# Optimization experiments

Measured on AMD Instinct MI355X. Metric: run time of the kernel, lower is better.

The kernel has to match this reference:

```python
import jax, jax.numpy as jnp
import numpy as np

DIM = 256
WS = 7
NUM_HEADS = 8
NW = 4096


def _relative_position_index(ws: int) -> jnp.ndarray:
    coords = jnp.stack(jnp.meshgrid(jnp.arange(ws), jnp.arange(ws), indexing='ij'))  # [2, ws, ws]
    flat = coords.reshape(2, -1)                                # [2, N]
    rel = flat[:, :, None] - flat[:, None, :]                   # [2, N, N]
    rel = rel.transpose(1, 2, 0) + (ws - 1)                     # [N, N, 2]
    rel = rel.at[:, :, 0].multiply(2 * ws - 1)
    return rel.sum(-1).astype(jnp.int32)                        # [N, N]


def setup_inputs() -> dict:
    key = jax.random.key(0)
    ks = jax.random.split(key, 7)
    N = WS * WS
    x_win = jax.random.normal(ks[0], (NW, N, DIM), dtype=jnp.float32)
    attn_mask = jnp.zeros((NW, N, N), dtype=jnp.float32)
    w_qkv = jax.random.normal(ks[1], (3 * DIM, DIM), dtype=jnp.float32) * (1.0 / np.sqrt(DIM))
    b_qkv = jax.random.normal(ks[2], (3 * DIM,), dtype=jnp.float32) * 0.02
    w_proj = jax.random.normal(ks[3], (DIM, DIM), dtype=jnp.float32) * (1.0 / np.sqrt(DIM))
    b_proj = jax.random.normal(ks[4], (DIM,), dtype=jnp.float32) * 0.02
    bias_table = jax.random.normal(ks[5], ((2 * WS - 1) * (2 * WS - 1), NUM_HEADS), dtype=jnp.float32)
    rel_index = _relative_position_index(WS)
    return {
        'x_win': x_win, 'attn_mask': attn_mask,
        'w_qkv': w_qkv, 'b_qkv': b_qkv,
        'w_proj': w_proj, 'b_proj': b_proj,
        'bias_table': bias_table, 'rel_index': rel_index,
    }


def reference(x_win, attn_mask, w_qkv, b_qkv, w_proj, b_proj, bias_table, rel_index):
    nW, N, C = x_win.shape
    H = bias_table.shape[-1]
    head_dim = C // H
    scale = 1.0 / np.sqrt(head_dim).astype(np.float32)

    # QKV projection (eqx.nn.Linear: y = W x + b)
    qkv = jnp.einsum('wnc,oc->wno', x_win, w_qkv) + b_qkv      # [nW, N, 3C]
    q, k, v = jnp.split(qkv, 3, axis=-1)

    def to_heads(t):
        return t.reshape(nW, N, H, head_dim).transpose(0, 2, 1, 3)  # [nW, H, N, d]

    q, k, v = to_heads(q), to_heads(k), to_heads(v)

    attn = jnp.einsum('whnd,whmd->whnm', q * scale, k)          # [nW, H, N, N]

    # Gathered relative position bias -> [H, N, N]
    bias = bias_table[rel_index.reshape(-1)].reshape(N, N, H).transpose(2, 0, 1)
    attn = attn + bias[None, :, :, :] + attn_mask[:, None, :, :]
    attn = jax.nn.softmax(attn, axis=-1)

    out = jnp.einsum('whnm,whmd->whnd', attn, v)                # [nW, H, N, d]
    out = out.transpose(0, 2, 1, 3).reshape(nW, N, C)
    out = jnp.einsum('wnc,oc->wno', out, w_proj) + b_proj
    return out
```

## Files before the change

kernel.cpp:

```cpp
#include <hip/hip_runtime.h>
#include <hip/hip_bf16.h>

typedef __bf16 bf16;
typedef bf16 bf16x4 __attribute__((ext_vector_type(4)));
typedef bf16 bf16x8 __attribute__((ext_vector_type(8)));
typedef float f32x4 __attribute__((ext_vector_type(4)));

#define MFMA16(a, b, c) __builtin_amdgcn_mfma_f32_16x16x32_bf16((a), (b), (c), 0, 0, 0)

constexpr int kN = 49, kC = 256;
constexpr float kScale = 0.17677669529663687f;

constexpr int WQKV_OFF = 0;
constexpr int WPROJ_OFF = 393216;
constexpr int BIAS_OFF = 524288;
constexpr int BQKV_OFF = 601120;

constexpr int XB_OFF = 0;
constexpr int QK_OFF = 25600;
constexpr int QS = 400;
constexpr int LDS_BYTES = 76800;

__global__ void prep_kernel(const float* __restrict__ w_qkv, const float* __restrict__ b_qkv,
                            const float* __restrict__ w_proj, const float* __restrict__ bias_table,
                            const int* __restrict__ rel_index, char* __restrict__ ws) {
  int i = blockIdx.x * 256 + threadIdx.x;
  bf16* wqkvb = (bf16*)(ws + WQKV_OFF);
  bf16* wprojb = (bf16*)(ws + WPROJ_OFF);
  float* biasx = (float*)(ws + BIAS_OFF);
  float* bqs = (float*)(ws + BQKV_OFF);
  if (i < 196608) {
    float v = w_qkv[i];
    if (i < 65536) v *= kScale;
    wqkvb[i] = (bf16)v;
  } else if (i < 262144) {
    int j = i - 196608;
    wprojb[j] = (bf16)w_proj[j];
  } else if (i < 281352) {
    int j = i - 262144;
    int h = j / 2401, nm = j - h * 2401;
    int mm = nm / 49, nn = nm - mm * 49;
    biasx[j] = bias_table[rel_index[nn * 49 + mm] * 8 + h];
  } else if (i < 282120) {
    int j = i - 281352;
    bqs[j] = b_qkv[j] * (j < 256 ? kScale : 1.0f);
  }
}

__global__ __launch_bounds__(256, 2) void attn_kernel(
    const float* __restrict__ x, const float* __restrict__ mask, const float* __restrict__ b_proj,
    const char* __restrict__ ws, float* __restrict__ out) {
  extern __shared__ char smem[];
  bf16* xb = (bf16*)(smem + XB_OFF);
  bf16* qk = (bf16*)(smem + QK_OFF);
  float* outf = (float*)(smem + QK_OFF);

  const bf16* wqkvb = (const bf16*)(ws + WQKV_OFF);
  const bf16* wprojb = (const bf16*)(ws + WPROJ_OFF);
  const float* biasx = (const float*)(ws + BIAS_OFF);
  const float* bqs = (const float*)(ws + BQKV_OFF);

  const int tid = threadIdx.x;
  const int w = blockIdx.x;
  const int lane = tid & 63;
  const int wave = tid >> 6;
  const int g = lane >> 4;
  const int c = lane & 15;

  const float* xw = x + (size_t)w * (kN * kC);

#pragma unroll
  for (int it = 0; it < 13; ++it) {
    int idx = it * 256 + tid;
    if (idx < 3136) {
      int n = idx >> 6, c4 = (idx & 63) << 2;
      float4 v = ((const float4*)xw)[idx];
      bf16x4 b4;
      b4[0] = (bf16)v.x; b4[1] = (bf16)v.y; b4[2] = (bf16)v.z; b4[3] = (bf16)v.w;
      *(bf16x4*)(xb + ((c4 >> 3) * QS + n * 8 + (c4 & 7))) = b4;
    }
  }
  __syncthreads();

  for (int t = 0; t < 8; ++t) {
    int ot = wave * 8 + t;
    const bf16* ab = wqkvb + (ot * 16 + c) * 256 + g * 8;
    bf16x8 afr[8];
#pragma unroll
    for (int ks = 0; ks < 8; ++ks) afr[ks] = *(const bf16x8*)(ab + ks * 32);
    f32x4 acc[4] = {};
#pragma unroll
    for (int ks = 0; ks < 8; ++ks) {
      const bf16* bb = xb + (ks * 4 + g) * QS + c * 8;
#pragma unroll
      for (int nt = 0; nt < 4; ++nt) {
        bf16x8 bfr = *(const bf16x8*)(bb + nt * 128);
        acc[nt] = MFMA16(afr[ks], bfr, acc[nt]);
      }
    }
    int ob = ot * 16 + g * 4;
    float bq0 = bqs[ob], bq1 = bqs[ob + 1], bq2 = bqs[ob + 2], bq3 = bqs[ob + 3];
    int oc = ob >> 3, olow = ob & 7;
#pragma unroll
    for (int nt = 0; nt < 4; ++nt) {
      int n = nt * 16 + c;
      if (n < 50) {
        bool ok = (n < 49);
        bf16x4 pk;
        pk[0] = ok ? (bf16)(acc[nt][0] + bq0) : (bf16)0.f;
        pk[1] = ok ? (bf16)(acc[nt][1] + bq1) : (bf16)0.f;
        pk[2] = ok ? (bf16)(acc[nt][2] + bq2) : (bf16)0.f;
        pk[3] = ok ? (bf16)(acc[nt][3] + bq3) : (bf16)0.f;
        *(bf16x4*)(qk + (oc * QS + n * 8 + olow)) = pk;
      }
    }
  }

  bf16x8 va[2][2][2];
  for (int t = 0; t < 4; ++t) {
    int ct = wave * 4 + t;
    int o = 512 + ct * 16 + c;
    const bf16* bb = wqkvb + o * 256 + g * 8;
    bf16x8 bfr[8];
#pragma unroll
    for (int ks = 0; ks < 8; ++ks) bfr[ks] = *(const bf16x8*)(bb + ks * 32);
    f32x4 acc[4] = {};
#pragma unroll
    for (int ks = 0; ks < 8; ++ks) {
      const bf16* abL = xb + (ks * 4 + g) * QS + c * 8;
#pragma unroll
      for (int mt = 0; mt < 4; ++mt) {
        bf16x8 afr = *(const bf16x8*)(abL + mt * 128);
        acc[mt] = MFMA16(afr, bfr[ks], acc[mt]);
      }
    }
    float bv = bqs[o];
#pragma unroll
    for (int mt = 0; mt < 4; ++mt) {
      acc[mt][0] += bv; acc[mt][1] += bv; acc[mt][2] += bv; acc[mt][3] += bv;
    }
    int hh = t >> 1, dt = t & 1;
    int base = ((g & 1) * 2) * 16 + c;
#pragma unroll
    for (int ks = 0; ks < 2; ++ks) {
      f32x4 aL = acc[2 * ks], aH = acc[2 * ks + 1];
      float e[8];
#pragma unroll
      for (int i = 0; i < 4; ++i) {
        float xA = __shfl(aL[i], base), yA = __shfl(aH[i], base);
        float xB = __shfl(aL[i], base + 16), yB = __shfl(aH[i], base + 16);
        e[i] = (g < 2) ? xA : yA;
        e[4 + i] = (g < 2) ? xB : yB;
      }
      bf16x8 f;
#pragma unroll
      for (int j = 0; j < 8; ++j) {
        int m = ks * 32 + g * 8 + j;
        f[j] = (m < 49) ? (bf16)e[j] : (bf16)0.f;
      }
      va[hh][dt][ks] = f;
    }
  }
  __syncthreads();

  const int h0 = wave * 2;
  const float* mk = mask + (size_t)w * 2401;

#pragma unroll
  for (int hh = 0; hh < 2; ++hh) {
    int h = h0 + hh;
    const float* bhT = biasx + h * 2401;

    bf16x8 qa[4], kb[4];
#pragma unroll
    for (int rt = 0; rt < 4; ++rt) {
      int n = rt * 16 + c; n = n > 49 ? 49 : n;
      qa[rt] = *(const bf16x8*)(qk + ((h * 4 + g) * QS + n * 8));
    }
#pragma unroll
    for (int mt = 0; mt < 4; ++mt) {
      int m = mt * 16 + c; m = m > 49 ? 49 : m;
      kb[mt] = *(const bf16x8*)(qk + ((32 + h * 4 + g) * QS + m * 8));
    }

    f32x4 s[4][4] = {};
#pragma unroll
    for (int mt = 0; mt < 4; ++mt)
#pragma unroll
      for (int nt = 0; nt < 4; ++nt) s[mt][nt] = MFMA16(kb[mt], qa[nt], s[mt][nt]);

    f32x4 oacc[2][4] = {};
#pragma unroll
    for (int nt = 0; nt < 4; ++nt) {
      int n = nt * 16 + c;
      int nc = n > 48 ? 48 : n;
      bool nok = (n < 49);
      float vals[4][4];
#pragma unroll
      for (int mt = 0; mt < 4; ++mt)
#pragma unroll
        for (int i = 0; i < 4; ++i) {
          int m = mt * 16 + g * 4 + i;
          int mc2 = m > 48 ? 48 : m;
          float bv = bhT[mc2 * 49 + nc];
          float mv = mk[nc * 49 + mc2];
          vals[mt][i] = (nok && m < 49) ? (s[mt][nt][i] + bv + mv) : -1e30f;
        }
      float mx = vals[0][0];
#pragma unroll
      for (int mt = 0; mt < 4; ++mt)
#pragma unroll
        for (int i = 0; i < 4; ++i) mx = fmaxf(mx, vals[mt][i]);
      mx = fmaxf(mx, __shfl_xor(mx, 16));
      mx = fmaxf(mx, __shfl_xor(mx, 32));
      float p_[4][4];
      float sum = 0.f;
#pragma unroll
      for (int mt = 0; mt < 4; ++mt)
#pragma unroll
        for (int i = 0; i < 4; ++i) {
          float pv = __expf(vals[mt][i] - mx);
          p_[mt][i] = pv;
          sum += pv;
        }
      sum += __shfl_xor(sum, 16);
      sum += __shfl_xor(sum, 32);
      float rinv = nok ? (1.0f / sum) : 0.0f;
#pragma unroll
      for (int mt = 0; mt < 4; ++mt)
#pragma unroll
        for (int i = 0; i < 4; ++i) p_[mt][i] *= rinv;

#pragma unroll
      for (int ks = 0; ks < 2; ++ks) {
        float e[8];
#pragma unroll
        for (int j = 0; j < 8; ++j) {
          int src = ((g & 1) * 2 + (j >> 2)) * 16 + c;
          float vA = __shfl(p_[2 * ks][j & 3], src);
          float vB = __shfl(p_[2 * ks + 1][j & 3], src);
          e[j] = (g < 2) ? vA : vB;
        }
        bf16x8 f;
#pragma unroll
        for (int j = 0; j < 8; ++j) f[j] = (bf16)e[j];
#pragma unroll
        for (int dt = 0; dt < 2; ++dt) oacc[dt][nt] = MFMA16(va[hh][dt][ks], f, oacc[dt][nt]);
      }
    }

#pragma unroll
    for (int dt = 0; dt < 2; ++dt) {
      int cb = h * 32 + dt * 16 + g * 4;
      int cc = cb >> 3, clow = cb & 7;
#pragma unroll
      for (int nt = 0; nt < 4; ++nt) {
        int n = nt * 16 + c;
        if (n < 49) {
          bf16x4 pk;
          pk[0] = (bf16)oacc[dt][nt][0]; pk[1] = (bf16)oacc[dt][nt][1];
          pk[2] = (bf16)oacc[dt][nt][2]; pk[3] = (bf16)oacc[dt][nt][3];
          *(bf16x4*)(xb + (cc * QS + n * 8 + clow)) = pk;
        }
      }
    }
  }
  __syncthreads();

  for (int t = 0; t < 4; ++t) {
    int ct = wave * 4 + t;
    const bf16* bb = wprojb + (ct * 16 + c) * 256 + g * 8;
    bf16x8 bfr[8];
#pragma unroll
    for (int ks = 0; ks < 8; ++ks) bfr[ks] = *(const bf16x8*)(bb + ks * 32);
    f32x4 acc[4] = {};
#pragma unroll
    for (int ks = 0; ks < 8; ++ks) {
      const bf16* abL = xb + (ks * 4 + g) * QS + c * 8;
#pragma unroll
      for (int mt = 0; mt < 4; ++mt) {
        bf16x8 afr = *(const bf16x8*)(abL + mt * 128);
        acc[mt] = MFMA16(afr, bfr[ks], acc[mt]);
      }
    }
    float bp = b_proj[ct * 16 + c];
    int co = ct * 16 + c, q = co >> 2, c3 = co & 3;
#pragma unroll
    for (int mt = 0; mt < 4; ++mt) {
#pragma unroll
      for (int i = 0; i < 4; ++i) {
        int n = mt * 16 + g * 4 + i;
        if (n < 49) outf[n * 256 + ((q ^ (n & 15)) << 2) + c3] = acc[mt][i] + bp;
      }
    }
  }
  __syncthreads();

  float4* outw4 = (float4*)(out + (size_t)w * (kN * kC));
  const float4* outf4 = (const float4*)outf;
#pragma unroll
  for (int it = 0; it < 13; ++it) {
    int f = it * 256 + tid;
    if (f < 3136) {
      int n = f >> 6, q = f & 63;
      outw4[f] = outf4[n * 64 + (q ^ (n & 15))];
    }
  }
}

extern "C" void kernel_launch(void* const* d_in, const int* in_sizes, int n_in,
                              void* d_out, int out_size, void* d_ws, size_t ws_size,
                              hipStream_t stream) {
  const float* x = (const float*)d_in[0];
  const float* mask = (const float*)d_in[1];
  const float* w_qkv = (const float*)d_in[2];
  const float* b_qkv = (const float*)d_in[3];
  const float* w_proj = (const float*)d_in[4];
  const float* b_proj = (const float*)d_in[5];
  const float* bias_table = (const float*)d_in[6];
  const int* rel_index = (const int*)d_in[7];
  float* out = (float*)d_out;
  char* ws = (char*)d_ws;

  (void)in_sizes; (void)n_in; (void)out_size; (void)ws_size;

  hipFuncSetAttribute((const void*)attn_kernel, hipFuncAttributeMaxDynamicSharedMemorySize,
                      LDS_BYTES);

  prep_kernel<<<1103, 256, 0, stream>>>(w_qkv, b_qkv, w_proj, bias_table, rel_index, ws);
  attn_kernel<<<4096, 256, LDS_BYTES, stream>>>(x, mask, b_proj, ws, out);
}
```

Before: 431.0 us.

## Fuse per-head QKV projection into attention to shrink LDS and raise occupancy

Each wave now computes the Q and K projections for its own heads directly into registers through lane shuffles, so Q/K never go through LDS. The attention output gets its own LDS buffer, and the output projection is staged in two column halves that reuse the x buffer. Together these cut LDS from 76.8KB to about 51KB, which allows the launch bound to rise from 2 to 3 blocks per CU. In exchange there is more register pressure, extra shuffles, and an additional pair of barriers in the output stage.

```diff
diff --git a/kernel.cpp b/kernel.cpp
--- a/kernel.cpp
+++ b/kernel.cpp
@@ -8,7 +8,6 @@
 
 #define MFMA16(a, b, c) __builtin_amdgcn_mfma_f32_16x16x32_bf16((a), (b), (c), 0, 0, 0)
 
-constexpr int kN = 49, kC = 256;
 constexpr float kScale = 0.17677669529663687f;
 
 constexpr int WQKV_OFF = 0;
@@ -16,10 +15,10 @@
 constexpr int BIAS_OFF = 524288;
 constexpr int BQKV_OFF = 601120;
 
-constexpr int XB_OFF = 0;
-constexpr int QK_OFF = 25600;
+constexpr int A_OFF = 0;
+constexpr int B_OFF = 25600;
 constexpr int QS = 400;
-constexpr int LDS_BYTES = 76800;
+constexpr int LDS_BYTES = 51456;
 
 __global__ void prep_kernel(const float* __restrict__ w_qkv, const float* __restrict__ b_qkv,
                             const float* __restrict__ w_proj, const float* __restrict__ bias_table,
@@ -47,13 +46,13 @@
   }
 }
 
-__global__ __launch_bounds__(256, 2) void attn_kernel(
+__global__ __launch_bounds__(256, 3) void attn_kernel(
     const float* __restrict__ x, const float* __restrict__ mask, const float* __restrict__ b_proj,
     const char* __restrict__ ws, float* __restrict__ out) {
   extern __shared__ char smem[];
-  bf16* xb = (bf16*)(smem + XB_OFF);
-  bf16* qk = (bf16*)(smem + QK_OFF);
-  float* outf = (float*)(smem + QK_OFF);
+  bf16* xb = (bf16*)(smem + A_OFF);
+  bf16* ao = (bf16*)(smem + B_OFF);
+  float* outf = (float*)(smem + A_OFF);
 
   const bf16* wqkvb = (const bf16*)(ws + WQKV_OFF);
   const bf16* wprojb = (const bf16*)(ws + WPROJ_OFF);
@@ -67,7 +66,7 @@
   const int g = lane >> 4;
   const int c = lane & 15;
 
-  const float* xw = x + (size_t)w * (kN * kC);
+  const float* xw = x + (size_t)w * 12544;
 
 #pragma unroll
   for (int it = 0; it < 13; ++it) {
@@ -82,119 +81,117 @@
   }
   __syncthreads();
 
-  for (int t = 0; t < 8; ++t) {
-    int ot = wave * 8 + t;
-    const bf16* ab = wqkvb + (ot * 16 + c) * 256 + g * 8;
-    bf16x8 afr[8];
-#pragma unroll
-    for (int ks = 0; ks < 8; ++ks) afr[ks] = *(const bf16x8*)(ab + ks * 32);
-    f32x4 acc[4] = {};
-#pragma unroll
-    for (int ks = 0; ks < 8; ++ks) {
-      const bf16* bb = xb + (ks * 4 + g) * QS + c * 8;
-#pragma unroll
-      for (int nt = 0; nt < 4; ++nt) {
-        bf16x8 bfr = *(const bf16x8*)(bb + nt * 128);
-        acc[nt] = MFMA16(afr[ks], bfr, acc[nt]);
-      }
-    }
-    int ob = ot * 16 + g * 4;
-    float bq0 = bqs[ob], bq1 = bqs[ob + 1], bq2 = bqs[ob + 2], bq3 = bqs[ob + 3];
-    int oc = ob >> 3, olow = ob & 7;
+  const float* mk = mask + (size_t)w * 2401;
+  const int h0 = wave * 2;
+
+  for (int hh = 0; hh < 2; ++hh) {
+    const int h = h0 + hh;
+
+    bf16x8 qa[4], kb[4];
+#pragma unroll
+    for (int qksel = 0; qksel < 2; ++qksel) {
+      const int obase = qksel * 256 + h * 32;
+      f32x4 acc2[2][4] = {};
+#pragma unroll
+      for (int tf = 0; tf < 2; ++tf) {
+        const bf16* abw = wqkvb + (obase + tf * 16 + c) * 256 + g * 8;
+        bf16x8 afr[8];
+#pragma unroll
+        for (int ks = 0; ks < 8; ++ks) afr[ks] = *(const bf16x8*)(abw + ks * 32);
+#pragma unroll
+        for (int ks = 0; ks < 8; ++ks) {
+          const bf16* bb = xb + (ks * 4 + g) * QS + c * 8;
+#pragma unroll
+          for (int nt = 0; nt < 4; ++nt) {
+            bf16x8 bfr = *(const bf16x8*)(bb + nt * 128);
+            acc2[tf][nt] = MFMA16(afr[ks], bfr, acc2[tf][nt]);
+          }
+        }
+#pragma unroll
+        for (int i = 0; i < 4; ++i) {
+          float bq = bqs[obase + tf * 16 + g * 4 + i];
+#pragma unroll
+          for (int nt = 0; nt < 4; ++nt) acc2[tf][nt][i] += bq;
+        }
+      }
+      const int base = (g & 1) * 32 + c;
+#pragma unroll
+      for (int rt = 0; rt < 4; ++rt) {
+        float e[8];
+#pragma unroll
+        for (int i = 0; i < 4; ++i) {
+          float a0 = __shfl(acc2[0][rt][i], base);
+          float a1 = __shfl(acc2[0][rt][i], base + 16);
+          float b0 = __shfl(acc2[1][rt][i], base);
+          float b1 = __shfl(acc2[1][rt][i], base + 16);
+          e[i] = (g < 2) ? a0 : b0;
+          e[i + 4] = (g < 2) ? a1 : b1;
+        }
+        bf16x8 f;
+#pragma unroll
+        for (int j = 0; j < 8; ++j) f[j] = (bf16)e[j];
+        if (qksel == 0) qa[rt] = f; else kb[rt] = f;
+      }
+    }
+
+    bf16x8 va[2][2];
+#pragma unroll
+    for (int dt = 0; dt < 2; ++dt) {
+      const int ct = wave * 4 + hh * 2 + dt;
+      const int o = 512 + ct * 16 + c;
+      const bf16* bbw = wqkvb + o * 256 + g * 8;
+      bf16x8 bfr[8];
+#pragma unroll
+      for (int ks = 0; ks < 8; ++ks) bfr[ks] = *(const bf16x8*)(bbw + ks * 32);
+      f32x4 acc[4] = {};
+#pragma unroll
+      for (int ks = 0; ks < 8; ++ks) {
+        const bf16* abL = xb + (ks * 4 + g) * QS + c * 8;
+#pragma unroll
+        for (int mt = 0; mt < 4; ++mt) {
+          bf16x8 afr = *(const bf16x8*)(abL + mt * 128);
+          acc[mt] = MFMA16(afr, bfr[ks], acc[mt]);
+        }
+      }
+      const float bv = bqs[o];
+#pragma unroll
+      for (int mt = 0; mt < 4; ++mt) {
+        acc[mt][0] += bv; acc[mt][1] += bv; acc[mt][2] += bv; acc[mt][3] += bv;
+      }
+      const int base = (g & 1) * 32 + c;
+#pragma unroll
+      for (int ks = 0; ks < 2; ++ks) {
+        float e[8];
+#pragma unroll
+        for (int i = 0; i < 4; ++i) {
+          float xA = __shfl(acc[2 * ks][i], base);
+          float yA = __shfl(acc[2 * ks + 1][i], base);
+          float xB = __shfl(acc[2 * ks][i], base + 16);
+          float yB = __shfl(acc[2 * ks + 1][i], base + 16);
+          e[i] = (g < 2) ? xA : yA;
+          e[i + 4] = (g < 2) ? xB : yB;
+        }
+        bf16x8 f;
+#pragma unroll
+        for (int j = 0; j < 8; ++j) {
+          int m = ks * 32 + g * 8 + j;
+          f[j] = (m < 49) ? (bf16)e[j] : (bf16)0.f;
+        }
+        va[dt][ks] = f;
+      }
+    }
+
+    const float* bhT = biasx + h * 2401;
+    f32x4 oacc[2][4] = {};
 #pragma unroll
     for (int nt = 0; nt < 4; ++nt) {
-      int n = nt * 16 + c;
-      if (n < 50) {
-        bool ok = (n < 49);
-        bf16x4 pk;
-        pk[0] = ok ? (bf16)(acc[nt][0] + bq0) : (bf16)0.f;
-        pk[1] = ok ? (bf16)(acc[nt][1] + bq1) : (bf16)0.f;
-        pk[2] = ok ? (bf16)(acc[nt][2] + bq2) : (bf16)0.f;
-        pk[3] = ok ? (bf16)(acc[nt][3] + bq3) : (bf16)0.f;
-        *(bf16x4*)(qk + (oc * QS + n * 8 + olow)) = pk;
-      }
-    }
-  }
-
-  bf16x8 va[2][2][2];
-  for (int t = 0; t < 4; ++t) {
-    int ct = wave * 4 + t;
-    int o = 512 + ct * 16 + c;
-    const bf16* bb = wqkvb + o * 256 + g * 8;
-    bf16x8 bfr[8];
-#pragma unroll
-    for (int ks = 0; ks < 8; ++ks) bfr[ks] = *(const bf16x8*)(bb + ks * 32);
-    f32x4 acc[4] = {};
-#pragma unroll
-    for (int ks = 0; ks < 8; ++ks) {
-      const bf16* abL = xb + (ks * 4 + g) * QS + c * 8;
-#pragma unroll
-      for (int mt = 0; mt < 4; ++mt) {
-        bf16x8 afr = *(const bf16x8*)(abL + mt * 128);
-        acc[mt] = MFMA16(afr, bfr[ks], acc[mt]);
-      }
-    }
-    float bv = bqs[o];
-#pragma unroll
-    for (int mt = 0; mt < 4; ++mt) {
-      acc[mt][0] += bv; acc[mt][1] += bv; acc[mt][2] += bv; acc[mt][3] += bv;
-    }
-    int hh = t >> 1, dt = t & 1;
-    int base = ((g & 1) * 2) * 16 + c;
-#pragma unroll
-    for (int ks = 0; ks < 2; ++ks) {
-      f32x4 aL = acc[2 * ks], aH = acc[2 * ks + 1];
-      float e[8];
-#pragma unroll
-      for (int i = 0; i < 4; ++i) {
-        float xA = __shfl(aL[i], base), yA = __shfl(aH[i], base);
-        float xB = __shfl(aL[i], base + 16), yB = __shfl(aH[i], base + 16);
-        e[i] = (g < 2) ? xA : yA;
-        e[4 + i] = (g < 2) ? xB : yB;
-      }
-      bf16x8 f;
-#pragma unroll
-      for (int j = 0; j < 8; ++j) {
-        int m = ks * 32 + g * 8 + j;
-        f[j] = (m < 49) ? (bf16)e[j] : (bf16)0.f;
-      }
-      va[hh][dt][ks] = f;
-    }
-  }
-  __syncthreads();
-
-  const int h0 = wave * 2;
-  const float* mk = mask + (size_t)w * 2401;
-
-#pragma unroll
-  for (int hh = 0; hh < 2; ++hh) {
-    int h = h0 + hh;
-    const float* bhT = biasx + h * 2401;
-
-    bf16x8 qa[4], kb[4];
-#pragma unroll
-    for (int rt = 0; rt < 4; ++rt) {
-      int n = rt * 16 + c; n = n > 49 ? 49 : n;
-      qa[rt] = *(const bf16x8*)(qk + ((h * 4 + g) * QS + n * 8));
-    }
-#pragma unroll
-    for (int mt = 0; mt < 4; ++mt) {
-      int m = mt * 16 + c; m = m > 49 ? 49 : m;
-      kb[mt] = *(const bf16x8*)(qk + ((32 + h * 4 + g) * QS + m * 8));
-    }
-
-    f32x4 s[4][4] = {};
-#pragma unroll
-    for (int mt = 0; mt < 4; ++mt)
-#pragma unroll
-      for (int nt = 0; nt < 4; ++nt) s[mt][nt] = MFMA16(kb[mt], qa[nt], s[mt][nt]);
-
-    f32x4 oacc[2][4] = {};
-#pragma unroll
-    for (int nt = 0; nt < 4; ++nt) {
-      int n = nt * 16 + c;
-      int nc = n > 48 ? 48 : n;
-      bool nok = (n < 49);
+      f32x4 z = {};
+      f32x4 sc[4];
+#pragma unroll
+      for (int mt = 0; mt < 4; ++mt) sc[mt] = MFMA16(kb[mt], qa[nt], z);
+      const int n = nt * 16 + c;
+      const int nc = n > 48 ? 48 : n;
+      const bool nok = (n < 49);
       float vals[4][4];
 #pragma unroll
       for (int mt = 0; mt < 4; ++mt)
@@ -204,7 +201,7 @@
           int mc2 = m > 48 ? 48 : m;
           float bv = bhT[mc2 * 49 + nc];
           float mv = mk[nc * 49 + mc2];
-          vals[mt][i] = (nok && m < 49) ? (s[mt][nt][i] + bv + mv) : -1e30f;
+          vals[mt][i] = (nok && m < 49) ? (sc[mt][i] + bv + mv) : -1e30f;
         }
       float mx = vals[0][0];
 #pragma unroll
@@ -245,7 +242,7 @@
 #pragma unroll
         for (int j = 0; j < 8; ++j) f[j] = (bf16)e[j];
 #pragma unroll
-        for (int dt = 0; dt < 2; ++dt) oacc[dt][nt] = MFMA16(va[hh][dt][ks], f, oacc[dt][nt]);
+        for (int dt = 0; dt < 2; ++dt) oacc[dt][nt] = MFMA16(va[dt][ks], f, oacc[dt][nt]);
       }
     }
 
@@ -260,51 +257,57 @@
           bf16x4 pk;
           pk[0] = (bf16)oacc[dt][nt][0]; pk[1] = (bf16)oacc[dt][nt][1];
           pk[2] = (bf16)oacc[dt][nt][2]; pk[3] = (bf16)oacc[dt][nt][3];
-          *(bf16x4*)(xb + (cc * QS + n * 8 + clow)) = pk;
+          *(bf16x4*)(ao + (cc * QS + n * 8 + clow)) = pk;
         }
       }
     }
   }
   __syncthreads();
 
-  for (int t = 0; t < 4; ++t) {
-    int ct = wave * 4 + t;
-    const bf16* bb = wprojb + (ct * 16 + c) * 256 + g * 8;
-    bf16x8 bfr[8];
-#pragma unroll
-    for (int ks = 0; ks < 8; ++ks) bfr[ks] = *(const bf16x8*)(bb + ks * 32);
-    f32x4 acc[4] = {};
-#pragma unroll
-    for (int ks = 0; ks < 8; ++ks) {
-      const bf16* abL = xb + (ks * 4 + g) * QS + c * 8;
+  float4* outw4 = (float4*)(out + (size_t)w * 12544);
+  const float4* outf4 = (const float4*)outf;
+#pragma unroll
+  for (int half = 0; half < 2; ++half) {
+#pragma unroll
+    for (int tt = 0; tt < 2; ++tt) {
+      const int ctl = wave * 2 + tt;
+      const int ct = half * 8 + ctl;
+      const bf16* bbw = wprojb + (ct * 16 + c) * 256 + g * 8;
+      bf16x8 bfr[8];
+#pragma unroll
+      for (int ks = 0; ks < 8; ++ks) bfr[ks] = *(const bf16x8*)(bbw + ks * 32);
+      f32x4 acc[4] = {};
+#pragma unroll
+      for (int ks = 0; ks < 8; ++ks) {
+        const bf16* abL = ao + (ks * 4 + g) * QS + c * 8;
+#pragma unroll
+        for (int mt = 0; mt < 4; ++mt) {
+          bf16x8 afr = *(const bf16x8*)(abL + mt * 128);
+          acc[mt] = MFMA16(afr, bfr[ks], acc[mt]);
+        }
+      }
+      float bp = b_proj[ct * 16 + c];
+      const int q = ctl * 4 + (c >> 2);
+      const int c3 = c & 3;
 #pragma unroll
       for (int mt = 0; mt < 4; ++mt) {
-        bf16x8 afr = *(const bf16x8*)(abL + mt * 128);
-        acc[mt] = MFMA16(afr, bfr[ks], acc[mt]);
-      }
-    }
-    float bp = b_proj[ct * 16 + c];
-    int co = ct * 16 + c, q = co >> 2, c3 = co & 3;
-#pragma unroll
-    for (int mt = 0; mt < 4; ++mt) {
-#pragma unroll
-      for (int i = 0; i < 4; ++i) {
-        int n = mt * 16 + g * 4 + i;
-        if (n < 49) outf[n * 256 + ((q ^ (n & 15)) << 2) + c3] = acc[mt][i] + bp;
-      }
-    }
-  }
-  __syncthreads();
-
-  float4* outw4 = (float4*)(out + (size_t)w * (kN * kC));
-  const float4* outf4 = (const float4*)outf;
-#pragma unroll
-  for (int it = 0; it < 13; ++it) {
-    int f = it * 256 + tid;
-    if (f < 3136) {
-      int n = f >> 6, q = f & 63;
-      outw4[f] = outf4[n * 64 + (q ^ (n & 15))];
-    }
+#pragma unroll
+        for (int i = 0; i < 4; ++i) {
+          int n = mt * 16 + g * 4 + i;
+          if (n < 49) outf[n * 128 + ((q ^ (n & 7)) << 2) + c3] = acc[mt][i] + bp;
+        }
+      }
+    }
+    __syncthreads();
+#pragma unroll
+    for (int it = 0; it < 7; ++it) {
+      int f = it * 256 + tid;
+      if (f < 1568) {
+        int n = f >> 5, q2 = f & 31;
+        outw4[n * 64 + half * 32 + q2] = outf4[n * 32 + (q2 ^ (n & 7))];
+      }
+    }
+    __syncthreads();
   }
 }
 
```

After: 811.4 us. +88.3%, slower.

## Register-tile projection GEMMs 4x4, pad LDS stride, prefetch bias/mask, drop softmax max

Applied to the files above, without the earlier changes.

The QKV, V and output projection loops are restructured so each wave keeps a 4x4 block of MFMA accumulators. Each LDS activation fragment and each weight fragment loaded per k-step is then reused across four output tiles instead of one. The LDS row stride is padded from 400 to 410 elements to change the bank mapping. The bias and mask gathers for the next query tile are issued ahead of the current tile's softmax. The softmax max-reduction is removed and exp is applied directly, which saves shuffles and a pass. The cost is more accumulator registers, possibly misaligned 16-byte LDS reads with the odd stride, and overflow risk for large logits.

```diff
diff --git a/kernel.cpp b/kernel.cpp
--- a/kernel.cpp
+++ b/kernel.cpp
@@ -8,7 +8,6 @@
 
 #define MFMA16(a, b, c) __builtin_amdgcn_mfma_f32_16x16x32_bf16((a), (b), (c), 0, 0, 0)
 
-constexpr int kN = 49, kC = 256;
 constexpr float kScale = 0.17677669529663687f;
 
 constexpr int WQKV_OFF = 0;
@@ -16,10 +15,9 @@
 constexpr int BIAS_OFF = 524288;
 constexpr int BQKV_OFF = 601120;
 
-constexpr int XB_OFF = 0;
-constexpr int QK_OFF = 25600;
-constexpr int QS = 400;
-constexpr int LDS_BYTES = 76800;
+constexpr int QK_OFF = 26240;
+constexpr int QS = 410;
+constexpr int LDS_BYTES = 78720;
 
 __global__ void prep_kernel(const float* __restrict__ w_qkv, const float* __restrict__ b_qkv,
                             const float* __restrict__ w_proj, const float* __restrict__ bias_table,
@@ -47,11 +45,25 @@
   }
 }
 
+__device__ __forceinline__ bf16x8 xpose8(f32x4 lo, f32x4 hi, int base, bool glow) {
+  bf16x8 f;
+#pragma unroll
+  for (int i = 0; i < 4; ++i) {
+    float a0 = __shfl(lo[i], base);
+    float a1 = __shfl(lo[i], base + 16);
+    float b0 = __shfl(hi[i], base);
+    float b1 = __shfl(hi[i], base + 16);
+    f[i] = (bf16)(glow ? a0 : b0);
+    f[i + 4] = (bf16)(glow ? a1 : b1);
+  }
+  return f;
+}
+
 __global__ __launch_bounds__(256, 2) void attn_kernel(
     const float* __restrict__ x, const float* __restrict__ mask, const float* __restrict__ b_proj,
     const char* __restrict__ ws, float* __restrict__ out) {
   extern __shared__ char smem[];
-  bf16* xb = (bf16*)(smem + XB_OFF);
+  bf16* xb = (bf16*)(smem);
   bf16* qk = (bf16*)(smem + QK_OFF);
   float* outf = (float*)(smem + QK_OFF);
 
@@ -67,7 +79,7 @@
   const int g = lane >> 4;
   const int c = lane & 15;
 
-  const float* xw = x + (size_t)w * (kN * kC);
+  const float* xw = x + (size_t)w * 12544;
 
 #pragma unroll
   for (int it = 0; it < 13; ++it) {
@@ -82,93 +94,94 @@
   }
   __syncthreads();
 
-  for (int t = 0; t < 8; ++t) {
-    int ot = wave * 8 + t;
-    const bf16* ab = wqkvb + (ot * 16 + c) * 256 + g * 8;
-    bf16x8 afr[8];
-#pragma unroll
-    for (int ks = 0; ks < 8; ++ks) afr[ks] = *(const bf16x8*)(ab + ks * 32);
-    f32x4 acc[4] = {};
+  for (int qd = 0; qd < 2; ++qd) {
+    const int ot0 = wave * 8 + qd * 4;
+    f32x4 acc[4][4] = {};
 #pragma unroll
     for (int ks = 0; ks < 8; ++ks) {
-      const bf16* bb = xb + (ks * 4 + g) * QS + c * 8;
+      bf16x8 b[4];
+#pragma unroll
+      for (int nt = 0; nt < 4; ++nt)
+        b[nt] = *(const bf16x8*)(xb + (ks * 4 + g) * QS + c * 8 + nt * 128);
+      bf16x8 a[4];
+#pragma unroll
+      for (int t = 0; t < 4; ++t)
+        a[t] = *(const bf16x8*)(wqkvb + ((ot0 + t) * 16 + c) * 256 + ks * 32 + g * 8);
+#pragma unroll
+      for (int t = 0; t < 4; ++t)
+#pragma unroll
+        for (int nt = 0; nt < 4; ++nt) acc[t][nt] = MFMA16(a[t], b[nt], acc[t][nt]);
+    }
+#pragma unroll
+    for (int t = 0; t < 4; ++t) {
+      const int ot = ot0 + t;
+      const int ob = ot * 16 + g * 4;
+      const float bq0 = bqs[ob], bq1 = bqs[ob + 1], bq2 = bqs[ob + 2], bq3 = bqs[ob + 3];
+      const int oc = ob >> 3, olow = ob & 7;
 #pragma unroll
       for (int nt = 0; nt < 4; ++nt) {
-        bf16x8 bfr = *(const bf16x8*)(bb + nt * 128);
-        acc[nt] = MFMA16(afr[ks], bfr, acc[nt]);
-      }
-    }
-    int ob = ot * 16 + g * 4;
-    float bq0 = bqs[ob], bq1 = bqs[ob + 1], bq2 = bqs[ob + 2], bq3 = bqs[ob + 3];
-    int oc = ob >> 3, olow = ob & 7;
-#pragma unroll
-    for (int nt = 0; nt < 4; ++nt) {
-      int n = nt * 16 + c;
-      if (n < 50) {
-        bool ok = (n < 49);
-        bf16x4 pk;
-        pk[0] = ok ? (bf16)(acc[nt][0] + bq0) : (bf16)0.f;
-        pk[1] = ok ? (bf16)(acc[nt][1] + bq1) : (bf16)0.f;
-        pk[2] = ok ? (bf16)(acc[nt][2] + bq2) : (bf16)0.f;
-        pk[3] = ok ? (bf16)(acc[nt][3] + bq3) : (bf16)0.f;
-        *(bf16x4*)(qk + (oc * QS + n * 8 + olow)) = pk;
-      }
-    }
-  }
+        int n = nt * 16 + c;
+        if (n < 50) {
+          bool ok = (n < 49);
+          bf16x4 pk;
+          pk[0] = ok ? (bf16)(acc[t][nt][0] + bq0) : (bf16)0.f;
+          pk[1] = ok ? (bf16)(acc[t][nt][1] + bq1) : (bf16)0.f;
+          pk[2] = ok ? (bf16)(acc[t][nt][2] + bq2) : (bf16)0.f;
+          pk[3] = ok ? (bf16)(acc[t][nt][3] + bq3) : (bf16)0.f;
+          *(bf16x4*)(qk + (oc * QS + n * 8 + olow)) = pk;
+        }
+      }
+    }
+  }
+
+  const int base = (g & 1) * 32 + c;
+  const bool glow = (g < 2);
 
   bf16x8 va[2][2][2];
-  for (int t = 0; t < 4; ++t) {
-    int ct = wave * 4 + t;
-    int o = 512 + ct * 16 + c;
-    const bf16* bb = wqkvb + o * 256 + g * 8;
-    bf16x8 bfr[8];
-#pragma unroll
-    for (int ks = 0; ks < 8; ++ks) bfr[ks] = *(const bf16x8*)(bb + ks * 32);
-    f32x4 acc[4] = {};
+  {
+    f32x4 acc[4][4] = {};
 #pragma unroll
     for (int ks = 0; ks < 8; ++ks) {
-      const bf16* abL = xb + (ks * 4 + g) * QS + c * 8;
+      bf16x8 a[4];
+#pragma unroll
+      for (int mt = 0; mt < 4; ++mt)
+        a[mt] = *(const bf16x8*)(xb + (ks * 4 + g) * QS + c * 8 + mt * 128);
+      bf16x8 bw[4];
+#pragma unroll
+      for (int t = 0; t < 4; ++t)
+        bw[t] = *(const bf16x8*)(wqkvb + (512 + (wave * 4 + t) * 16 + c) * 256 + ks * 32 + g * 8);
+#pragma unroll
+      for (int t = 0; t < 4; ++t)
+#pragma unroll
+        for (int mt = 0; mt < 4; ++mt) acc[t][mt] = MFMA16(a[mt], bw[t], acc[t][mt]);
+    }
+#pragma unroll
+    for (int t = 0; t < 4; ++t) {
+      const int o = 512 + (wave * 4 + t) * 16 + c;
+      const float bv = bqs[o];
 #pragma unroll
       for (int mt = 0; mt < 4; ++mt) {
-        bf16x8 afr = *(const bf16x8*)(abL + mt * 128);
-        acc[mt] = MFMA16(afr, bfr[ks], acc[mt]);
-      }
-    }
-    float bv = bqs[o];
-#pragma unroll
-    for (int mt = 0; mt < 4; ++mt) {
-      acc[mt][0] += bv; acc[mt][1] += bv; acc[mt][2] += bv; acc[mt][3] += bv;
-    }
-    int hh = t >> 1, dt = t & 1;
-    int base = ((g & 1) * 2) * 16 + c;
-#pragma unroll
-    for (int ks = 0; ks < 2; ++ks) {
-      f32x4 aL = acc[2 * ks], aH = acc[2 * ks + 1];
-      float e[8];
-#pragma unroll
-      for (int i = 0; i < 4; ++i) {
-        float xA = __shfl(aL[i], base), yA = __shfl(aH[i], base);
-        float xB = __shfl(aL[i], base + 16), yB = __shfl(aH[i], base + 16);
-        e[i] = (g < 2) ? xA : yA;
-        e[4 + i] = (g < 2) ? xB : yB;
-      }
-      bf16x8 f;
-#pragma unroll
-      for (int j = 0; j < 8; ++j) {
-        int m = ks * 32 + g * 8 + j;
-        f[j] = (m < 49) ? (bf16)e[j] : (bf16)0.f;
-      }
-      va[hh][dt][ks] = f;
+        acc[t][mt][0] += bv; acc[t][mt][1] += bv; acc[t][mt][2] += bv; acc[t][mt][3] += bv;
+      }
+#pragma unroll
+      for (int ks = 0; ks < 2; ++ks) {
+        bf16x8 f = xpose8(acc[t][2 * ks], acc[t][2 * ks + 1], base, glow);
+#pragma unroll
+        for (int j = 0; j < 8; ++j) {
+          int m = ks * 32 + g * 8 + j;
+          if (m >= 49) f[j] = (bf16)0.f;
+        }
+        va[t >> 1][t & 1][ks] = f;
+      }
     }
   }
   __syncthreads();
 
-  const int h0 = wave * 2;
   const float* mk = mask + (size_t)w * 2401;
 
 #pragma unroll
   for (int hh = 0; hh < 2; ++hh) {
-    int h = h0 + hh;
+    const int h = wave * 2 + hh;
     const float* bhT = biasx + h * 2401;
 
     bf16x8 qa[4], kb[4];
@@ -189,38 +202,36 @@
 #pragma unroll
       for (int nt = 0; nt < 4; ++nt) s[mt][nt] = MFMA16(kb[mt], qa[nt], s[mt][nt]);
 
+    float bi[16], mi[16];
+#define GATHER(NT)                                              \
+    {                                                           \
+      const int n_ = (NT) * 16 + c;                             \
+      const int nc_ = n_ > 48 ? 48 : n_;                        \
+      _Pragma("unroll") for (int mt = 0; mt < 4; ++mt)          \
+        _Pragma("unroll") for (int i = 0; i < 4; ++i) {         \
+          int m_ = mt * 16 + g * 4 + i;                         \
+          int mc_ = m_ > 48 ? 48 : m_;                          \
+          bi[mt * 4 + i] = bhT[mc_ * 49 + nc_];                 \
+          mi[mt * 4 + i] = mk[nc_ * 49 + mc_];                  \
+        }                                                       \
+    }
+
+    GATHER(0);
     f32x4 oacc[2][4] = {};
 #pragma unroll
     for (int nt = 0; nt < 4; ++nt) {
-      int n = nt * 16 + c;
-      int nc = n > 48 ? 48 : n;
-      bool nok = (n < 49);
-      float vals[4][4];
+      const int n = nt * 16 + c;
+      const bool nok = (n < 49);
+      float p[4][4];
+      float sum = 0.f;
 #pragma unroll
       for (int mt = 0; mt < 4; ++mt)
 #pragma unroll
         for (int i = 0; i < 4; ++i) {
           int m = mt * 16 + g * 4 + i;
-          int mc2 = m > 48 ? 48 : m;
-          float bv = bhT[mc2 * 49 + nc];
-          float mv = mk[nc * 49 + mc2];
-          vals[mt][i] = (nok && m < 49) ? (s[mt][nt][i] + bv + mv) : -1e30f;
-        }
-      float mx = vals[0][0];
-#pragma unroll
-      for (int mt = 0; mt < 4; ++mt)
-#pragma unroll
-        for (int i = 0; i < 4; ++i) mx = fmaxf(mx, vals[mt][i]);
-      mx = fmaxf(mx, __shfl_xor(mx, 16));
-      mx = fmaxf(mx, __shfl_xor(mx, 32));
-      float p_[4][4];
-      float sum = 0.f;
-#pragma unroll
-      for (int mt = 0; mt < 4; ++mt)
-#pragma unroll
-        for (int i = 0; i < 4; ++i) {
-          float pv = __expf(vals[mt][i] - mx);
-          p_[mt][i] = pv;
+          float v = s[mt][nt][i] + bi[mt * 4 + i] + mi[mt * 4 + i];
+          float pv = (nok && m < 49) ? __expf(v) : 0.f;
+          p[mt][i] = pv;
           sum += pv;
         }
       sum += __shfl_xor(sum, 16);
@@ -229,25 +240,29 @@
 #pragma unroll
       for (int mt = 0; mt < 4; ++mt)
 #pragma unroll
-        for (int i = 0; i < 4; ++i) p_[mt][i] *= rinv;
+        for (int i = 0; i < 4; ++i) p[mt][i] *= rinv;
+
+      if (nt < 3) {
+        if (nt == 0) GATHER(1);
+        if (nt == 1) GATHER(2);
+        if (nt == 2) GATHER(3);
+      }
 
 #pragma unroll
       for (int ks = 0; ks < 2; ++ks) {
-        float e[8];
+        bf16x8 f;
 #pragma unroll
         for (int j = 0; j < 8; ++j) {
           int src = ((g & 1) * 2 + (j >> 2)) * 16 + c;
-          float vA = __shfl(p_[2 * ks][j & 3], src);
-          float vB = __shfl(p_[2 * ks + 1][j & 3], src);
-          e[j] = (g < 2) ? vA : vB;
-        }
-        bf16x8 f;
-#pragma unroll
-        for (int j = 0; j < 8; ++j) f[j] = (bf16)e[j];
+          float vA = __shfl(p[2 * ks][j & 3], src);
+          float vB = __shfl(p[2 * ks + 1][j & 3], src);
+          f[j] = (bf16)(glow ? vA : vB);
+        }
 #pragma unroll
         for (int dt = 0; dt < 2; ++dt) oacc[dt][nt] = MFMA16(va[hh][dt][ks], f, oacc[dt][nt]);
       }
     }
+#undef GATHER
 
 #pragma unroll
     for (int dt = 0; dt < 2; ++dt) {
@@ -267,36 +282,41 @@
   }
   __syncthreads();
 
-  for (int t = 0; t < 4; ++t) {
-    int ct = wave * 4 + t;
-    const bf16* bb = wprojb + (ct * 16 + c) * 256 + g * 8;
-    bf16x8 bfr[8];
-#pragma unroll
-    for (int ks = 0; ks < 8; ++ks) bfr[ks] = *(const bf16x8*)(bb + ks * 32);
-    f32x4 acc[4] = {};
+  {
+    f32x4 acc[4][4] = {};
 #pragma unroll
     for (int ks = 0; ks < 8; ++ks) {
-      const bf16* abL = xb + (ks * 4 + g) * QS + c * 8;
+      bf16x8 a[4];
+#pragma unroll
+      for (int mt = 0; mt < 4; ++mt)
+        a[mt] = *(const bf16x8*)(xb + (ks * 4 + g) * QS + c * 8 + mt * 128);
+      bf16x8 bw[4];
+#pragma unroll
+      for (int t = 0; t < 4; ++t)
+        bw[t] = *(const bf16x8*)(wprojb + ((wave * 4 + t) * 16 + c) * 256 + ks * 32 + g * 8);
+#pragma unroll
+      for (int t = 0; t < 4; ++t)
+#pragma unroll
+        for (int mt = 0; mt < 4; ++mt) acc[t][mt] = MFMA16(a[mt], bw[t], acc[t][mt]);
+    }
+#pragma unroll
+    for (int t = 0; t < 4; ++t) {
+      const int ct = wave * 4 + t;
+      const float bp = b_proj[ct * 16 + c];
+      const int co = ct * 16 + c, q = co >> 2, c3 = co & 3;
 #pragma unroll
       for (int mt = 0; mt < 4; ++mt) {
-        bf16x8 afr = *(const bf16x8*)(abL + mt * 128);
-        acc[mt] = MFMA16(afr, bfr[ks], acc[mt]);
-      }
-    }
-    float bp = b_proj[ct * 16 + c];
-    int co = ct * 16 + c, q = co >> 2, c3 = co & 3;
-#pragma unroll
-    for (int mt = 0; mt < 4; ++mt) {
-#pragma unroll
-      for (int i = 0; i < 4; ++i) {
-        int n = mt * 16 + g * 4 + i;
-        if (n < 49) outf[n * 256 + ((q ^ (n & 15)) << 2) + c3] = acc[mt][i] + bp;
+#pragma unroll
+        for (int i = 0; i < 4; ++i) {
+          int n = mt * 16 + g * 4 + i;
+          if (n < 49) outf[n * 256 + ((q ^ (n & 15)) << 2) + c3] = acc[t][mt][i] + bp;
+        }
       }
     }
   }
   __syncthreads();
 
-  float4* outw4 = (float4*)(out + (size_t)w * (kN * kC));
+  float4* outw4 = (float4*)(out + (size_t)w * 12544);
   const float4* outf4 = (const float4*)outf;
 #pragma unroll
   for (int it = 0; it < 13; ++it) {
```

Result: slower. 443.9 us (+3.0%).
